# Kernel tuning notes

Measured on AMD Instinct MI355X. Metric: run time of the kernel, lower is better.

The kernel has to match this reference:

```python
import jax, jax.numpy as jnp
import numpy as np

KEEP_ID, DEL_ID, PAD_ID, STOP_ID, ANNO_ID = 1, 2, 0, 102, 103
V, E, H = 21128, 768, 768
B, T = 8, 256
S = T + 1  # org/simp length; S = T+1 guarantees counters never go out of range


def setup_inputs() -> dict:
    key = jax.random.key(0)
    ks = jax.random.split(key, 16)
    def p(i, shape, scale):
        return jax.random.normal(ks[i], shape, jnp.float32) * scale
    return {
        "input_edits": jax.random.randint(ks[0], (B, T), 0, V),
        "org_ids": jax.random.randint(ks[1], (B, S), 0, V),
        "simp_sent": jax.random.randint(ks[2], (B, S), 0, V),
        "h0": jax.random.normal(ks[3], (B, H), jnp.float32),
        "c0": jax.random.normal(ks[4], (B, H), jnp.float32),
        "encoder_outputs_org": jax.random.normal(ks[5], (B, S, E), jnp.float32),
        "emb": p(6, (V, E), 0.02),
        "Wih_e": p(7, (4 * H, E), 0.03), "Whh_e": p(8, (4 * H, H), 0.03), "b_e": jnp.zeros((4 * H,), jnp.float32),
        "Wih_w": p(9, (4 * H, E), 0.03), "Whh_w": p(10, (4 * H, H), 0.03), "b_w": jnp.zeros((4 * H,), jnp.float32),
        "W_attn": p(11, (H, H), 0.03),
        "W_align": p(12, (H, E), 0.03),
        "W_mlp": p(13, (E, 4 * H), 0.03), "b_mlp": jnp.zeros((E,), jnp.float32),
        "W_out": p(14, (V, E), 0.02), "b_out": jnp.zeros((V,), jnp.float32),
    }


def lstm(x, h0, c0, Wih, Whh, b):
    # x: [B,T,E]; single-layer batch_first LSTM, torch gate order (i,f,g,o)
    def step(carry, xt):
        h, c = carry
        g = xt @ Wih.T + h @ Whh.T + b
        i, f, gg, o = jnp.split(g, 4, axis=-1)
        c2 = jax.nn.sigmoid(f) * c + jax.nn.sigmoid(i) * jnp.tanh(gg)
        h2 = jax.nn.sigmoid(o) * jnp.tanh(c2)
        return (h2, c2), h2
    (hT, cT), hs = jax.lax.scan(step, (h0, c0), jnp.swapaxes(x, 0, 1))
    return jnp.swapaxes(hs, 0, 1), hT, cT


def reference(input_edits, org_ids, simp_sent, h0, c0, encoder_outputs_org,
              emb, Wih_e, Whh_e, b_e, Wih_w, Whh_w, b_w,
              W_attn, W_align, W_mlp, b_mlp, W_out, b_out):
    bsz, nsteps = input_edits.shape
    enc = jnp.tanh(encoder_outputs_org @ W_align.T)            # [B,S,H]
    out_edits, hT, cT = lstm(emb[input_edits], h0, c0, Wih_e, Whh_e, b_e)  # [B,T,H]
    out_words, _, _ = lstm(emb[simp_sent], h0, c0, Wih_w, Whh_w, b_w)      # [B,S,H]

    key = out_edits @ W_attn.T                                  # [B,T,H]
    attn = jax.nn.softmax(jnp.einsum('bth,bsh->bts', key, enc), axis=-1)
    ctx = jnp.einsum('bts,bsh->bth', attn, enc)                 # [B,T,H]

    # counter recurrence (pre-update counters are used for the gathers at step t)
    gold = jnp.swapaxes(input_edits[:, 1:], 0, 1)               # [T-1, B]
    bidx = jnp.arange(bsz)

    def cstep(carry, a):
        kd, ki, an = carry
        kd2 = kd + ((a == KEEP_ID) | (a == DEL_ID)).astype(kd.dtype)
        not_special = (a != DEL_ID) & (a != STOP_ID) & (a != PAD_ID)
        ki2 = ki + not_special.astype(ki.dtype)
        is_ins = not_special & (a != KEEP_ID)
        next_is_anno = org_ids[bidx, an + 1] == ANNO_ID
        an2 = jnp.where(is_ins & next_is_anno, an + 1, jnp.maximum(kd2, an))
        return (kd2, ki2, an2), (ki, an)

    z = jnp.zeros((bsz,), jnp.int32)
    _, (ki_seq, an_seq) = jax.lax.scan(cstep, (z, z, z), gold)
    ki_bt = jnp.swapaxes(ki_seq, 0, 1)                          # [B,T-1]
    an_bt = jnp.swapaxes(an_seq, 0, 1)                          # [B,T-1]

    c = jnp.take_along_axis(enc, an_bt[:, :, None], axis=1)        # [B,T-1,H]
    c_word = jnp.take_along_axis(out_words, ki_bt[:, :, None], axis=1)  # [B,T-1,H]

    Tm1 = nsteps - 1
    feat = jnp.concatenate([out_edits[:, :Tm1], ctx[:, :Tm1], c, c_word], axis=-1)  # [B,T-1,4H]
    mlp = jnp.tanh(feat @ W_mlp.T + b_mlp)                      # [B,T-1,E]
    logp = jax.nn.log_softmax(mlp @ W_out.T + b_out, axis=-1)   # [B,T-1,V]
    return logp, hT, cT
```

## Files before the change

kernel.cpp:

```cpp
#include <hip/hip_runtime.h>
#include <hip/hip_bf16.h>

typedef short s16x8 __attribute__((ext_vector_type(8)));
typedef float f32x4 __attribute__((ext_vector_type(4)));
typedef unsigned short u16;
typedef unsigned short u16x4 __attribute__((ext_vector_type(4)));
typedef unsigned long long u64;
typedef unsigned long long u64x2 __attribute__((ext_vector_type(2)));

__device__ __forceinline__ u16 f2bf(float f) {
  __hip_bfloat16 h = __float2bfloat16(f);
  u16 u;
  __builtin_memcpy(&u, &h, sizeof(u));
  return u;
}
__device__ __forceinline__ float bf2f(u16 u) {
  unsigned int x = ((unsigned int)u) << 16;
  float f;
  __builtin_memcpy(&f, &x, 4);
  return f;
}

__device__ __forceinline__ unsigned int a_ld32(const unsigned int* p) {
  return __hip_atomic_load(p, __ATOMIC_RELAXED, __HIP_MEMORY_SCOPE_AGENT);
}
__device__ __forceinline__ u64 a_ld64(const u64* p) {
  return __hip_atomic_load(p, __ATOMIC_RELAXED, __HIP_MEMORY_SCOPE_AGENT);
}
__device__ __forceinline__ void a_st32(unsigned int* p, unsigned int v) {
  __hip_atomic_store(p, v, __ATOMIC_RELAXED, __HIP_MEMORY_SCOPE_AGENT);
}

__device__ __forceinline__ void gload16(const void* g, void* l) {
  __builtin_amdgcn_global_load_lds(
      (const __attribute__((address_space(1))) unsigned int*)g,
      (__attribute__((address_space(3))) unsigned int*)l, 16, 0, 0);
}

template<int CBF16, int GATHER, int TANHA, int BIAS>
__global__ __launch_bounds__(256) void gemm_bt(
    const u16* __restrict__ A, const u16* __restrict__ B,
    const float* __restrict__ bias, void* __restrict__ Cv,
    const int* __restrict__ ids,
    int M, int N, int K, int lda, int ldb, int ldc,
    long sAz, long sBz, long sCz, int rpb, long cbs,
    const int* __restrict__ ids2, const float* __restrict__ bias2, int dM)
{
  __shared__ u16 sA[4096];
  __shared__ u16 sB[4096];
  const int tid = threadIdx.x;
  const int z = blockIdx.z;
  if (z) {
    if (dM) M += dM;
    if (ids2) ids = ids2;
    if (bias2) bias = bias2;
  }
  const int m0 = blockIdx.y * 128, n0 = blockIdx.x * 128;
  const u16* Ab = A + z * sAz;
  const u16* Bb = B + z * sBz;
  const int w = tid >> 6, lane = tid & 63;
  const int wr = w >> 1, wc = w & 1;
  const int lr = lane & 15, lk = lane >> 4;
  f32x4 acc[4][4] = {};
  const int e0 = tid * 8, e1 = e0 + 2048;
  const int r0 = e0 >> 5, c0 = e0 & 31;
  const int r1 = e1 >> 5, c1 = e1 & 31;
  long arow0, arow1;
  if (GATHER) {
    int i0 = m0 + r0; if (i0 >= M) i0 = M - 1;
    int i1 = m0 + r1; if (i1 >= M) i1 = M - 1;
    arow0 = (long)ids[i0] * lda;
    arow1 = (long)ids[i1] * lda;
  } else {
    arow0 = (long)(m0 + r0) * lda;
    arow1 = (long)(m0 + r1) * lda;
  }
  const long brow0 = (long)(n0 + r0) * ldb;
  const long brow1 = (long)(n0 + r1) * ldb;
  char* sAc = (char*)sA;
  char* sBc = (char*)sB;
  const size_t cb = (size_t)w * 1024;
  for (int kt = 0; kt < K; kt += 32) {
    __syncthreads();
    gload16(Ab + arow0 + kt + c0, sAc + cb);
    gload16(Ab + arow1 + kt + c1, sAc + 4096 + cb);
    gload16(Bb + brow0 + kt + c0, sBc + cb);
    gload16(Bb + brow1 + kt + c1, sBc + 4096 + cb);
    __syncthreads();
    s16x8 af[4], bf[4];
#pragma unroll
    for (int i = 0; i < 4; i++) {
      af[i] = *(const s16x8*)&sA[(wr*64 + i*16 + lr)*32 + lk*8];
      bf[i] = *(const s16x8*)&sB[(wc*64 + i*16 + lr)*32 + lk*8];
    }
#pragma unroll
    for (int mi = 0; mi < 4; mi++)
#pragma unroll
      for (int ni = 0; ni < 4; ni++)
        acc[mi][ni] = __builtin_amdgcn_mfma_f32_16x16x32_bf16(af[mi], bf[ni], acc[mi][ni], 0, 0, 0);
  }
#pragma unroll
  for (int mi = 0; mi < 4; mi++) {
#pragma unroll
    for (int ni = 0; ni < 4; ni++) {
#pragma unroll
      for (int r = 0; r < 4; r++) {
        int gm = m0 + wr*64 + mi*16 + lk*4 + r;
        int gn = n0 + wc*64 + ni*16 + lr;
        if (gm < M && gn < N) {
          float v = acc[mi][ni][r];
          if (BIAS) v += bias[gn];
          if (TANHA) v = tanhf(v);
          long ci = z * sCz + (long)(gm / rpb) * cbs + (long)(gm % rpb) * ldc + gn;
          if (CBF16) ((u16*)Cv)[ci] = f2bf(v);
          else       ((float*)Cv)[ci] = v;
        }
      }
    }
  }
}

__global__ __launch_bounds__(256) void cast_all(
    const float* __restrict__ emb, u16* __restrict__ emb_bf,
    const float* __restrict__ Wout, u16* __restrict__ Wout_bf,
    const float* __restrict__ Wihe, u16* __restrict__ Wihe_bf,
    const float* __restrict__ Wihw, u16* __restrict__ Wihw_bf,
    const float* __restrict__ Wmlp, u16* __restrict__ Wmlp_bf,
    const float* __restrict__ Walign, u16* __restrict__ Walign_bf,
    const float* __restrict__ Wattn, u16* __restrict__ Wattn_bf,
    const float* __restrict__ encoder, u16* __restrict__ encd_bf,
    const int* __restrict__ input_edits, const int* __restrict__ org_ids,
    int* __restrict__ ki_bt, int* __restrict__ an_bt,
    unsigned int* __restrict__ tags)
{
  int r = blockIdx.x;
  if (r == 53000) {
    int b = threadIdx.x;
    tags[b] = 0;
    if (b >= 8) return;
    int kd = 0, ki = 0, an = 0;
    for (int t = 0; t < 255; t++) {
      int a = input_edits[b * 256 + t + 1];
      ki_bt[b * 255 + t] = ki;
      an_bt[b * 255 + t] = an;
      int kd2 = kd + ((a == 1) || (a == 2) ? 1 : 0);
      int ns = (a != 2) && (a != 102) && (a != 0);
      int ki2 = ki + (ns ? 1 : 0);
      int is_ins = ns && (a != 1);
      int nia = (org_ids[b * 257 + an + 1] == 103);
      int mx = (kd2 > an) ? kd2 : an;
      int an2 = (is_ins && nia) ? (an + 1) : mx;
      kd = kd2; ki = ki2; an = an2;
    }
    return;
  }
  const float* src; u16* dst; int srows, cols;
  if (r < 21128)                    { src=emb;    dst=emb_bf;    srows=21128; cols=768; }
  else if ((r -= 21128) < 21248)    { src=Wout;   dst=Wout_bf;   srows=21128; cols=768; }
  else if ((r -= 21248) < 3072)     { src=Wihe;   dst=Wihe_bf;   srows=3072;  cols=768; }
  else if ((r -= 3072) < 3072)      { src=Wihw;   dst=Wihw_bf;   srows=3072;  cols=768; }
  else if ((r -= 3072) < 768)       { src=Wmlp;   dst=Wmlp_bf;   srows=768;   cols=3072; }
  else if ((r -= 768) < 768)        { src=Walign; dst=Walign_bf; srows=768;   cols=768; }
  else if ((r -= 768) < 768)        { src=Wattn;  dst=Wattn_bf;  srows=768;   cols=768; }
  else { r -= 768;                    src=encoder; dst=encd_bf;  srows=2056;  cols=768; }
  for (int c = threadIdx.x; c < cols; c += 256) {
    float v = (r < srows) ? src[(long)r * cols + c] : 0.f;
    dst[(long)r * cols + c] = f2bf(v);
  }
}

__global__ __launch_bounds__(256, 1) void lstm_persist(
    const float* __restrict__ Whh_e, const float* __restrict__ Whh_w,
    const float* __restrict__ xW_e, const float* __restrict__ xW_w,
    const float* __restrict__ h0, const float* __restrict__ c0,
    u16* __restrict__ hglob, unsigned int* __restrict__ tags,
    u16* __restrict__ out_e, u16* __restrict__ out_w,
    float* __restrict__ out_tail)
{
  const int wg = blockIdx.x;
  const int l = wg / 24, grp = wg % 24;
  const int u0 = grp * 32;
  const int tid = threadIdx.x;
  const int w = tid >> 6, lane = tid & 63;
  const int c16 = lane & 15, half = lane >> 4;
  const int uh = w >> 1, g0 = (w & 1) * 2;

  __shared__ u16 ldsh[12288];
  __shared__ float Gbuf[16][4][2][16];

  s16x8 wfrag[2][24];
  {
    const float* Wbase = l ? Whh_w : Whh_e;
#pragma unroll
    for (int g = 0; g < 2; g++) {
      const float* Wsrc = Wbase + (long)((g0 + g) * 768 + u0 + uh * 16 + c16) * 768 + half * 8;
#pragma unroll
      for (int s = 0; s < 24; s++) {
        float4 f0 = *(const float4*)(Wsrc + s * 32);
        float4 f1 = *(const float4*)(Wsrc + s * 32 + 4);
        s16x8 v;
        v[0]=f2bf(f0.x); v[1]=f2bf(f0.y); v[2]=f2bf(f0.z); v[3]=f2bf(f0.w);
        v[4]=f2bf(f1.x); v[5]=f2bf(f1.y); v[6]=f2bf(f1.z); v[7]=f2bf(f1.w);
        wfrag[g][s] = v;
      }
    }
  }

  const int ub = tid >> 4, j2 = (tid & 15) * 2;
  const int uA = u0 + j2;
  float creg0 = 0.f, creg1 = 0.f;
  if (tid < 128) {
    creg0 = c0[ub * 768 + uA];
    creg1 = c0[ub * 768 + uA + 1];
  }

  u16* hg = hglob + l * 24576;
  unsigned int* tg = tags + l * 64;
  const int swA = uA ^ ((ub & 7) << 3);

  if (tid < 128) {
    float v0 = h0[ub * 768 + uA], v1 = h0[ub * 768 + uA + 1];
    u16 h0a = f2bf(v0), h0b = f2bf(v1);
    u16 l0a = f2bf(v0 - bf2f(h0a)), l0b = f2bf(v1 - bf2f(h0b));
    a_st32((unsigned int*)&hg[ub * 768 + swA],
           (unsigned int)h0a | ((unsigned int)h0b << 16));
    a_st32((unsigned int*)&hg[(ub + 8) * 768 + swA],
           (unsigned int)l0a | ((unsigned int)l0b << 16));
  }
  __syncthreads();
  if (tid == 0) a_st32(&tg[grp], 1u);

  const int trow = l ? 257 : 256;
  const float* xrb = (l ? xW_w : xW_e) + ((long)ub * trow) * 3072 + uA;
  u16* outp = (l ? out_w : out_e) + (long)ub * 256 * 768 + uA;
  float2 xq0, xq1, xq2, xq3;
  if (tid < 128) {
    xq0 = *(const float2*)&xrb[0];
    xq1 = *(const float2*)&xrb[768];
    xq2 = *(const float2*)&xrb[1536];
    xq3 = *(const float2*)&xrb[2304];
  }

  for (int t = 0; t < 256; t++) {
    float2 nx0, nx1, nx2, nx3;
    if (tid < 128) {
      const float* xn = xrb + (long)(t + 1) * 3072;
      nx0 = *(const float2*)&xn[0];
      nx1 = *(const float2*)&xn[768];
      nx2 = *(const float2*)&xn[1536];
      nx3 = *(const float2*)&xn[2304];
    }

    {
      const unsigned int tgt = (unsigned int)(t + 1);
      const unsigned int* tp = tg + (t & 1) * 32;
      const bool need = (lane < 24) && (lane != grp);
      while (true) {
        unsigned int v = need ? a_ld32(&tp[lane]) : tgt;
        if (!__any(v < tgt)) break;
        __builtin_amdgcn_s_sleep(1);
      }
      asm volatile("" ::: "memory");
    }

    {
      const u64* hs8 = (const u64*)(hg + (t & 1) * 12288);
#pragma unroll
      for (int i = 0; i < 6; i++) {
        const int idx = i * 256 + tid;
        u64 a = a_ld64(&hs8[idx * 2 + 0]);
        u64 b = a_ld64(&hs8[idx * 2 + 1]);
        u64x2 vv; vv[0] = a; vv[1] = b;
        *(u64x2*)&ldsh[idx * 8] = vv;
      }
    }
    __syncthreads();

    f32x4 acc0 = {}, acc1 = {};
#pragma unroll
    for (int s = 0; s < 24; s++) {
      const int off = (c16 * 768 + s * 32 + half * 8) ^ ((c16 & 7) << 3);
      s16x8 a = *(const s16x8*)&ldsh[off];
      acc0 = __builtin_amdgcn_mfma_f32_16x16x32_bf16(a, wfrag[0][s], acc0, 0, 0, 0);
      acc1 = __builtin_amdgcn_mfma_f32_16x16x32_bf16(a, wfrag[1][s], acc1, 0, 0, 0);
    }
#pragma unroll
    for (int r = 0; r < 4; r++) {
      Gbuf[half * 4 + r][g0 + 0][uh][c16] = acc0[r];
      Gbuf[half * 4 + r][g0 + 1][uh][c16] = acc1[r];
    }
    __syncthreads();

    unsigned int hip = 0;
    float h20 = 0.f, h21 = 0.f, c20 = 0.f, c21 = 0.f;
    if (tid < 128) {
      const int uh0 = j2 >> 4, uc0 = j2 & 15;
      const int uc1 = (j2 + 1) & 15;
      float gi0 = Gbuf[ub][0][uh0][uc0] + Gbuf[ub + 8][0][uh0][uc0] + xq0.x;
      float gf0 = Gbuf[ub][1][uh0][uc0] + Gbuf[ub + 8][1][uh0][uc0] + xq1.x;
      float gg0 = Gbuf[ub][2][uh0][uc0] + Gbuf[ub + 8][2][uh0][uc0] + xq2.x;
      float go0 = Gbuf[ub][3][uh0][uc0] + Gbuf[ub + 8][3][uh0][uc0] + xq3.x;
      float gi1 = Gbuf[ub][0][uh0][uc1] + Gbuf[ub + 8][0][uh0][uc1] + xq0.y;
      float gf1 = Gbuf[ub][1][uh0][uc1] + Gbuf[ub + 8][1][uh0][uc1] + xq1.y;
      float gg1 = Gbuf[ub][2][uh0][uc1] + Gbuf[ub + 8][2][uh0][uc1] + xq2.y;
      float go1 = Gbuf[ub][3][uh0][uc1] + Gbuf[ub + 8][3][uh0][uc1] + xq3.y;
      float si0 = 1.f / (1.f + expf(-gi0)), si1 = 1.f / (1.f + expf(-gi1));
      float sf0 = 1.f / (1.f + expf(-gf0)), sf1 = 1.f / (1.f + expf(-gf1));
      float so0 = 1.f / (1.f + expf(-go0)), so1 = 1.f / (1.f + expf(-go1));
      c20 = sf0 * creg0 + si0 * tanhf(gg0);
      c21 = sf1 * creg1 + si1 * tanhf(gg1);
      h20 = so0 * tanhf(c20);
      h21 = so1 * tanhf(c21);
      creg0 = c20; creg1 = c21;
      u16 hiA = f2bf(h20), hiB = f2bf(h21);
      u16 loA = f2bf(h20 - bf2f(hiA)), loB = f2bf(h21 - bf2f(hiB));
      hip = (unsigned int)hiA | ((unsigned int)hiB << 16);
      unsigned int lop = (unsigned int)loA | ((unsigned int)loB << 16);
      u16* hb = hg + ((t + 1) & 1) * 12288;
      a_st32((unsigned int*)&hb[ub * 768 + swA], hip);
      a_st32((unsigned int*)&hb[(ub + 8) * 768 + swA], lop);
      xq0 = nx0; xq1 = nx1; xq2 = nx2; xq3 = nx3;
    }
    __syncthreads();
    if (tid == 0)
      a_st32(&tg[((t + 1) & 1) * 32 + grp], (unsigned int)(t + 2));

    if (tid < 128) {
      *(unsigned int*)&outp[(long)t * 768] = hip;
      if (l == 0 && t == 255) {
        *(float2*)&out_tail[43101120 + ub * 768 + uA] = make_float2(h20, h21);
        *(float2*)&out_tail[43107264 + ub * 768 + uA] = make_float2(c20, c21);
      }
    }
  }
}

__global__ __launch_bounds__(256) void softmax_k(
    const float* __restrict__ scores, u16* __restrict__ attn)
{
  const int row = blockIdx.x;
  const float* src = scores + (long)row * 288;
  u16* dst = attn + (long)row * 288;
  const int tid = threadIdx.x;
  float v0 = (tid < 257) ? src[tid] : -1e30f;
  float v1 = (tid + 256 < 257) ? src[tid + 256] : -1e30f;
  float mx = fmaxf(v0, v1);
  for (int o = 32; o; o >>= 1) mx = fmaxf(mx, __shfl_xor(mx, o));
  __shared__ float sm[4];
  __shared__ float ss[4];
  if ((tid & 63) == 0) sm[tid >> 6] = mx;
  __syncthreads();
  mx = fmaxf(fmaxf(sm[0], sm[1]), fmaxf(sm[2], sm[3]));
  float e0 = (tid < 257) ? expf(v0 - mx) : 0.f;
  float e1 = (tid + 256 < 257) ? expf(v1 - mx) : 0.f;
  float s = e0 + e1;
  for (int o = 32; o; o >>= 1) s += __shfl_xor(s, o);
  if ((tid & 63) == 0) ss[tid >> 6] = s;
  __syncthreads();
  s = ss[0] + ss[1] + ss[2] + ss[3];
  float inv = 1.f / s;
  dst[tid] = f2bf(e0 * inv);
  if (tid + 256 < 288) dst[tid + 256] = f2bf(e1 * inv);
}

__global__ __launch_bounds__(256) void transpose_enc(
    const u16* __restrict__ enc, u16* __restrict__ encT)
{
  __shared__ u16 tile[32][33];
  const int b = blockIdx.z, h0 = blockIdx.y * 32, s0 = blockIdx.x * 32;
  const int tx = threadIdx.x & 31, ty = threadIdx.x >> 5;
#pragma unroll
  for (int i = 0; i < 32; i += 8) {
    int s = s0 + ty + i;
    u16 v = (s < 257) ? enc[((long)b * 384 + s) * 768 + h0 + tx] : (u16)0;
    tile[ty + i][tx] = v;
  }
  __syncthreads();
#pragma unroll
  for (int i = 0; i < 32; i += 8) {
    int h = h0 + ty + i;
    encT[((long)b * 768 + h) * 288 + s0 + tx] = tile[tx][ty + i];
  }
}

__global__ __launch_bounds__(256) void feat_k(
    const u16* __restrict__ oute, const u16* __restrict__ ctx,
    const u16* __restrict__ encb, const u16* __restrict__ outw,
    const int* __restrict__ ki_bt, const int* __restrict__ an_bt,
    u16* __restrict__ feat)
{
  int q = blockIdx.x * 256 + threadIdx.x;
  int m = q / 768, qq = q - m * 768;
  int seg = qq / 192, off = (qq - seg * 192) * 4;
  u16x4 v = {0, 0, 0, 0};
  if (m < 2040) {
    int b = m / 255, t = m - b * 255;
    const u16* src;
    if (seg == 0)      src = oute + ((long)(b * 256 + t)) * 768 + off;
    else if (seg == 1) src = ctx  + ((long)(b * 256 + t)) * 768 + off;
    else if (seg == 2) src = encb + ((long)(b * 384 + an_bt[m])) * 768 + off;
    else               src = outw + ((long)(b * 256 + ki_bt[m])) * 768 + off;
    v = *(const u16x4*)src;
  }
  *(u16x4*)(feat + (long)q * 4) = v;
}

__global__ __launch_bounds__(256) void logsoftmax_k(float* __restrict__ logits)
{
  const int m = blockIdx.x;
  float* row = logits + (long)m * 21128;
  const int tid = threadIdx.x;
  float mx = -1e30f, sm = 0.f;
  for (int i = tid * 4; i < 21128; i += 1024) {
    float4 v = *(const float4*)(row + i);
    float m4 = fmaxf(fmaxf(v.x, v.y), fmaxf(v.z, v.w));
    if (m4 > mx) { sm *= expf(mx - m4); mx = m4; }
    sm += expf(v.x - mx) + expf(v.y - mx) + expf(v.z - mx) + expf(v.w - mx);
  }
  for (int o = 32; o; o >>= 1) {
    float mo = __shfl_xor(mx, o), so = __shfl_xor(sm, o);
    float nm = fmaxf(mx, mo);
    sm = sm * expf(mx - nm) + so * expf(mo - nm);
    mx = nm;
  }
  __shared__ float wm[4], wsum[4];
  __shared__ float srs;
  if ((tid & 63) == 0) { wm[tid >> 6] = mx; wsum[tid >> 6] = sm; }
  __syncthreads();
  if (tid == 0) {
    float M = wm[0], S = wsum[0];
    for (int i = 1; i < 4; i++) {
      float nm = fmaxf(M, wm[i]);
      S = S * expf(M - nm) + wsum[i] * expf(wm[i] - nm);
      M = nm;
    }
    srs = M + logf(S);
  }
  __syncthreads();
  const float rs = srs;
  for (int i = tid * 4; i < 21128; i += 1024) {
    float4 v = *(const float4*)(row + i);
    v.x -= rs; v.y -= rs; v.z -= rs; v.w -= rs;
    *(float4*)(row + i) = v;
  }
}

extern "C" void kernel_launch(void* const* d_in, const int* in_sizes, int n_in,
                              void* d_out, int out_size, void* d_ws, size_t ws_size,
                              hipStream_t stream) {
  (void)in_sizes; (void)n_in; (void)out_size; (void)ws_size;
  const int*   input_edits = (const int*)d_in[0];
  const int*   org_ids     = (const int*)d_in[1];
  const int*   simp_sent   = (const int*)d_in[2];
  const float* h0      = (const float*)d_in[3];
  const float* c0      = (const float*)d_in[4];
  const float* encoder = (const float*)d_in[5];
  const float* emb     = (const float*)d_in[6];
  const float* Wih_e   = (const float*)d_in[7];
  const float* Whh_e   = (const float*)d_in[8];
  const float* b_e     = (const float*)d_in[9];
  const float* Wih_w   = (const float*)d_in[10];
  const float* Whh_w   = (const float*)d_in[11];
  const float* b_w     = (const float*)d_in[12];
  const float* W_attn  = (const float*)d_in[13];
  const float* W_align = (const float*)d_in[14];
  const float* W_mlp   = (const float*)d_in[15];
  const float* b_mlp   = (const float*)d_in[16];
  const float* W_out   = (const float*)d_in[17];
  const float* b_out   = (const float*)d_in[18];

  float* out = (float*)d_out;
  float* xW_e = out;
  float* xW_w = out + 2048L * 3072;
  u16* emb_bf  = (u16*)(out + 2048L * 3072 + 2056L * 3072);
  u16* encd_bf = emb_bf + 21128L * 768;
  u16* feat_bf = encd_bf + 2176L * 768;

  char* p = (char*)d_ws;
  auto alloc = [&](size_t bytes) -> char* {
    char* r = p; p += (bytes + 255) & ~(size_t)255; return r;
  };
  u16* Wout_bf   = (u16*)alloc(21248L * 768 * 2);
  u16* Wihe_bf   = (u16*)alloc(3072L * 768 * 2);
  u16* Wihw_bf   = (u16*)alloc(3072L * 768 * 2);
  u16* Wmlp_bf   = (u16*)alloc(768L * 3072 * 2);
  u16* Walign_bf = (u16*)alloc(768L * 768 * 2);
  u16* Wattn_bf  = (u16*)alloc(768L * 768 * 2);
  u16* enc_bf    = (u16*)alloc(8L * 384 * 768 * 2);
  u16* encT_bf   = (u16*)alloc(8L * 768 * 288 * 2);
  u16* oute_bf   = (u16*)alloc(2048L * 768 * 2);
  u16* outw_bf   = (u16*)alloc(2048L * 768 * 2);
  u16* key_bf    = (u16*)alloc(2048L * 768 * 2);
  u16* attn_bf   = (u16*)alloc(8L * 256 * 288 * 2);
  u16* ctx_bf    = (u16*)alloc(2048L * 768 * 2);
  u16* mlp_bf    = (u16*)alloc(2048L * 768 * 2);
  float* scores  = (float*)alloc(8L * 256 * 288 * 4);
  u16* hglob     = (u16*)alloc(2L * 2 * 12288 * 2);
  unsigned int* tags = (unsigned int*)alloc(256 * 4);
  int* ki_bt     = (int*)alloc(2040 * 4);
  int* an_bt     = (int*)alloc(2040 * 4);

  dim3 blk(256);
  const int BIGR = 1 << 30;

  cast_all<<<53001, blk, 0, stream>>>(emb, emb_bf, W_out, Wout_bf,
                                      Wih_e, Wihe_bf, Wih_w, Wihw_bf,
                                      W_mlp, Wmlp_bf, W_align, Walign_bf,
                                      W_attn, Wattn_bf, encoder, encd_bf,
                                      input_edits, org_ids, ki_bt, an_bt, tags);

  gemm_bt<1, 0, 1, 0><<<dim3(6, 17, 1), blk, 0, stream>>>(
      encd_bf, Walign_bf, nullptr, enc_bf, nullptr,
      2056, 768, 768, 768, 768, 768, 0, 0, 0, 257, 294912L,
      nullptr, nullptr, 0);

  gemm_bt<0, 1, 0, 1><<<dim3(24, 17, 2), blk, 0, stream>>>(
      emb_bf, Wihe_bf, b_e, xW_e, input_edits,
      2048, 3072, 768, 768, 768, 3072, 0, 2359296L, 6291456L, BIGR, 0,
      simp_sent, b_w, 8);

  lstm_persist<<<48, blk, 0, stream>>>(
      Whh_e, Whh_w, xW_e, xW_w, h0, c0, hglob, tags,
      oute_bf, outw_bf, out);

  gemm_bt<1, 0, 0, 0><<<dim3(6, 16, 1), blk, 0, stream>>>(
      oute_bf, Wattn_bf, nullptr, key_bf, nullptr,
      2048, 768, 768, 768, 768, 768, 0, 0, 0, BIGR, 0,
      nullptr, nullptr, 0);
  gemm_bt<0, 0, 0, 0><<<dim3(3, 2, 8), blk, 0, stream>>>(
      key_bf, enc_bf, nullptr, scores, nullptr,
      256, 257, 768, 768, 768, 288, 196608L, 294912L, 73728L, BIGR, 0,
      nullptr, nullptr, 0);
  softmax_k<<<2048, blk, 0, stream>>>(scores, attn_bf);
  transpose_enc<<<dim3(9, 24, 8), blk, 0, stream>>>(enc_bf, encT_bf);
  gemm_bt<1, 0, 0, 0><<<dim3(6, 2, 8), blk, 0, stream>>>(
      attn_bf, encT_bf, nullptr, ctx_bf, nullptr,
      256, 768, 288, 288, 288, 768, 73728L, 221184L, 196608L, BIGR, 0,
      nullptr, nullptr, 0);

  feat_k<<<6144, blk, 0, stream>>>(oute_bf, ctx_bf, enc_bf, outw_bf,
                                   ki_bt, an_bt, feat_bf);
  gemm_bt<1, 0, 1, 1><<<dim3(6, 16, 1), blk, 0, stream>>>(
      feat_bf, Wmlp_bf, b_mlp, mlp_bf, nullptr,
      2040, 768, 3072, 3072, 3072, 768, 0, 0, 0, BIGR, 0,
      nullptr, nullptr, 0);
  gemm_bt<0, 0, 0, 1><<<dim3(166, 16, 1), blk, 0, stream>>>(
      mlp_bf, Wout_bf, b_out, out, nullptr,
      2040, 21128, 768, 768, 768, 21128, 0, 0, 0, BIGR, 0,
      nullptr, nullptr, 0);

  logsoftmax_k<<<2040, blk, 0, stream>>>(out);
}
```

Baseline: 1.706 ms.

## Overlap weight casts with LSTM and gather embeddings instead of casting full table

Result: faster. 1.661 ms (-2.6%).

```diff
diff --git a/kernel.cpp b/kernel.cpp
--- a/kernel.cpp
+++ b/kernel.cpp
@@ -37,7 +37,7 @@
       (__attribute__((address_space(3))) unsigned int*)l, 16, 0, 0);
 }
 
-template<int CBF16, int GATHER, int TANHA, int BIAS>
+template<int CBF16, int GATHER, int TANHA, int BIAS, int SWAPXY>
 __global__ __launch_bounds__(256) void gemm_bt(
     const u16* __restrict__ A, const u16* __restrict__ B,
     const float* __restrict__ bias, void* __restrict__ Cv,
@@ -55,7 +55,8 @@
     if (ids2) ids = ids2;
     if (bias2) bias = bias2;
   }
-  const int m0 = blockIdx.y * 128, n0 = blockIdx.x * 128;
+  const int m0 = (SWAPXY ? blockIdx.x : blockIdx.y) * 128;
+  const int n0 = (SWAPXY ? blockIdx.y : blockIdx.x) * 128;
   const u16* Ab = A + z * sAz;
   const u16* Bb = B + z * sBz;
   const int w = tid >> 6, lane = tid & 63;
@@ -120,21 +121,20 @@
   }
 }
 
-__global__ __launch_bounds__(256) void cast_all(
-    const float* __restrict__ emb, u16* __restrict__ emb_bf,
-    const float* __restrict__ Wout, u16* __restrict__ Wout_bf,
+__global__ __launch_bounds__(256) void cast_pre(
+    const float* __restrict__ emb,
     const float* __restrict__ Wihe, u16* __restrict__ Wihe_bf,
     const float* __restrict__ Wihw, u16* __restrict__ Wihw_bf,
-    const float* __restrict__ Wmlp, u16* __restrict__ Wmlp_bf,
     const float* __restrict__ Walign, u16* __restrict__ Walign_bf,
-    const float* __restrict__ Wattn, u16* __restrict__ Wattn_bf,
     const float* __restrict__ encoder, u16* __restrict__ encd_bf,
-    const int* __restrict__ input_edits, const int* __restrict__ org_ids,
+    u16* __restrict__ gath_bf,
+    const int* __restrict__ input_edits, const int* __restrict__ simp_sent,
+    const int* __restrict__ org_ids,
     int* __restrict__ ki_bt, int* __restrict__ an_bt,
     unsigned int* __restrict__ tags)
 {
   int r = blockIdx.x;
-  if (r == 53000) {
+  if (r == 13312) {
     int b = threadIdx.x;
     tags[b] = 0;
     if (b >= 8) return;
@@ -154,18 +154,18 @@
     }
     return;
   }
-  const float* src; u16* dst; int srows, cols;
-  if (r < 21128)                    { src=emb;    dst=emb_bf;    srows=21128; cols=768; }
-  else if ((r -= 21128) < 21248)    { src=Wout;   dst=Wout_bf;   srows=21128; cols=768; }
-  else if ((r -= 21248) < 3072)     { src=Wihe;   dst=Wihe_bf;   srows=3072;  cols=768; }
-  else if ((r -= 3072) < 3072)      { src=Wihw;   dst=Wihw_bf;   srows=3072;  cols=768; }
-  else if ((r -= 3072) < 768)       { src=Wmlp;   dst=Wmlp_bf;   srows=768;   cols=3072; }
-  else if ((r -= 768) < 768)        { src=Walign; dst=Walign_bf; srows=768;   cols=768; }
-  else if ((r -= 768) < 768)        { src=Wattn;  dst=Wattn_bf;  srows=768;   cols=768; }
-  else { r -= 768;                    src=encoder; dst=encd_bf;  srows=2056;  cols=768; }
+  const float* src; u16* dst; int valid, cols;
+  if (r < 3072)                   { src=Wihe + (long)r*768;   dst=Wihe_bf + (long)r*768;   valid=1; cols=768; }
+  else if ((r -= 3072) < 3072)    { src=Wihw + (long)r*768;   dst=Wihw_bf + (long)r*768;   valid=1; cols=768; }
+  else if ((r -= 3072) < 768)     { src=Walign + (long)r*768; dst=Walign_bf + (long)r*768; valid=1; cols=768; }
+  else if ((r -= 768) < 2176)     { src=encoder + (long)r*768; dst=encd_bf + (long)r*768;  valid=(r<2056); cols=768; }
+  else if ((r -= 2176) < 2048)    { src=emb + (long)input_edits[r]*768; dst=gath_bf + (long)r*768; valid=1; cols=768; }
+  else { r -= 2048;                 int ok=(r<2056);
+                                    src=emb + (ok ? (long)simp_sent[r]*768 : 0); 
+                                    dst=gath_bf + (long)(2048+r)*768; valid=ok; cols=768; }
   for (int c = threadIdx.x; c < cols; c += 256) {
-    float v = (r < srows) ? src[(long)r * cols + c] : 0.f;
-    dst[(long)r * cols + c] = f2bf(v);
+    float v = valid ? src[c] : 0.f;
+    dst[c] = f2bf(v);
   }
 }
 
@@ -175,18 +175,71 @@
     const float* __restrict__ h0, const float* __restrict__ c0,
     u16* __restrict__ hglob, unsigned int* __restrict__ tags,
     u16* __restrict__ out_e, u16* __restrict__ out_w,
-    float* __restrict__ out_tail)
+    float* __restrict__ out_tail,
+    const float* __restrict__ Wout, u16* __restrict__ Wout_bf,
+    const float* __restrict__ Wmlp, u16* __restrict__ Wmlp_bf,
+    const float* __restrict__ Wattn, u16* __restrict__ Wattn_bf,
+    const u16* __restrict__ enc_bf, u16* __restrict__ encT_bf)
 {
   const int wg = blockIdx.x;
+  const int tid = threadIdx.x;
+
+  __shared__ u16 ldsh[12288];
+  __shared__ float Gbuf[16][4][2][16];
+
+  if (wg >= 48) {
+    const int swg = wg - 48;
+    u16 (*tile)[33] = (u16(*)[33])ldsh;
+    const int TOT = 21248 + 768 + 768 + 1728;
+    for (int u = swg; u < TOT; u += 208) {
+      if (u < 21248) {
+        const float* src = Wout + (long)u * 768;
+        u16* dst = Wout_bf + (long)u * 768;
+        bool ok = (u < 21128);
+        for (int c = tid; c < 768; c += 256)
+          dst[c] = f2bf(ok ? src[c] : 0.f);
+      } else if (u < 22016) {
+        int r = u - 21248;
+        const float* src = Wmlp + (long)r * 3072;
+        u16* dst = Wmlp_bf + (long)r * 3072;
+        for (int c = tid; c < 3072; c += 256)
+          dst[c] = f2bf(src[c]);
+      } else if (u < 22784) {
+        int r = u - 22016;
+        const float* src = Wattn + (long)r * 768;
+        u16* dst = Wattn_bf + (long)r * 768;
+        for (int c = tid; c < 768; c += 256)
+          dst[c] = f2bf(src[c]);
+      } else {
+        int tau = u - 22784;
+        int s0 = (tau % 9) * 32;
+        int rem = tau / 9;
+        int hh0 = (rem % 24) * 32;
+        int b = rem / 24;
+        const int tx = tid & 31, ty = tid >> 5;
+#pragma unroll
+        for (int i = 0; i < 32; i += 8) {
+          int s = s0 + ty + i;
+          u16 v = (s < 257) ? enc_bf[((long)b * 384 + s) * 768 + hh0 + tx] : (u16)0;
+          tile[ty + i][tx] = v;
+        }
+        __syncthreads();
+#pragma unroll
+        for (int i = 0; i < 32; i += 8) {
+          int h = hh0 + ty + i;
+          encT_bf[((long)b * 768 + h) * 288 + s0 + tx] = tile[tx][ty + i];
+        }
+        __syncthreads();
+      }
+    }
+    return;
+  }
+
   const int l = wg / 24, grp = wg % 24;
   const int u0 = grp * 32;
-  const int tid = threadIdx.x;
   const int w = tid >> 6, lane = tid & 63;
   const int c16 = lane & 15, half = lane >> 4;
   const int uh = w >> 1, g0 = (w & 1) * 2;
-
-  __shared__ u16 ldsh[12288];
-  __shared__ float Gbuf[16][4][2][16];
 
   s16x8 wfrag[2][24];
   {
@@ -363,26 +416,6 @@
   if (tid + 256 < 288) dst[tid + 256] = f2bf(e1 * inv);
 }
 
-__global__ __launch_bounds__(256) void transpose_enc(
-    const u16* __restrict__ enc, u16* __restrict__ encT)
-{
-  __shared__ u16 tile[32][33];
-  const int b = blockIdx.z, h0 = blockIdx.y * 32, s0 = blockIdx.x * 32;
-  const int tx = threadIdx.x & 31, ty = threadIdx.x >> 5;
-#pragma unroll
-  for (int i = 0; i < 32; i += 8) {
-    int s = s0 + ty + i;
-    u16 v = (s < 257) ? enc[((long)b * 384 + s) * 768 + h0 + tx] : (u16)0;
-    tile[ty + i][tx] = v;
-  }
-  __syncthreads();
-#pragma unroll
-  for (int i = 0; i < 32; i += 8) {
-    int h = h0 + ty + i;
-    encT[((long)b * 768 + h) * 288 + s0 + tx] = tile[tx][ty + i];
-  }
-}
-
 __global__ __launch_bounds__(256) void feat_k(
     const u16* __restrict__ oute, const u16* __restrict__ ctx,
     const u16* __restrict__ encb, const u16* __restrict__ outw,
@@ -472,8 +505,7 @@
   float* out = (float*)d_out;
   float* xW_e = out;
   float* xW_w = out + 2048L * 3072;
-  u16* emb_bf  = (u16*)(out + 2048L * 3072 + 2056L * 3072);
-  u16* encd_bf = emb_bf + 21128L * 768;
+  u16* encd_bf = (u16*)(out + 2048L * 3072 + 2056L * 3072);
   u16* feat_bf = encd_bf + 2176L * 768;
 
   char* p = (char*)d_ws;
@@ -486,6 +518,7 @@
   u16* Wmlp_bf   = (u16*)alloc(768L * 3072 * 2);
   u16* Walign_bf = (u16*)alloc(768L * 768 * 2);
   u16* Wattn_bf  = (u16*)alloc(768L * 768 * 2);
+  u16* gath_bf   = (u16*)alloc(4224L * 768 * 2);
   u16* enc_bf    = (u16*)alloc(8L * 384 * 768 * 2);
   u16* encT_bf   = (u16*)alloc(8L * 768 * 288 * 2);
   u16* oute_bf   = (u16*)alloc(2048L * 768 * 2);
@@ -503,48 +536,47 @@
   dim3 blk(256);
   const int BIGR = 1 << 30;
 
-  cast_all<<<53001, blk, 0, stream>>>(emb, emb_bf, W_out, Wout_bf,
-                                      Wih_e, Wihe_bf, Wih_w, Wihw_bf,
-                                      W_mlp, Wmlp_bf, W_align, Walign_bf,
-                                      W_attn, Wattn_bf, encoder, encd_bf,
-                                      input_edits, org_ids, ki_bt, an_bt, tags);
-
-  gemm_bt<1, 0, 1, 0><<<dim3(6, 17, 1), blk, 0, stream>>>(
+  cast_pre<<<13313, blk, 0, stream>>>(emb, Wih_e, Wihe_bf, Wih_w, Wihw_bf,
+                                      W_align, Walign_bf, encoder, encd_bf,
+                                      gath_bf, input_edits, simp_sent,
+                                      org_ids, ki_bt, an_bt, tags);
+
+  gemm_bt<1, 0, 1, 0, 0><<<dim3(6, 17, 1), blk, 0, stream>>>(
       encd_bf, Walign_bf, nullptr, enc_bf, nullptr,
       2056, 768, 768, 768, 768, 768, 0, 0, 0, 257, 294912L,
       nullptr, nullptr, 0);
 
-  gemm_bt<0, 1, 0, 1><<<dim3(24, 17, 2), blk, 0, stream>>>(
-      emb_bf, Wihe_bf, b_e, xW_e, input_edits,
-      2048, 3072, 768, 768, 768, 3072, 0, 2359296L, 6291456L, BIGR, 0,
-      simp_sent, b_w, 8);
-
-  lstm_persist<<<48, blk, 0, stream>>>(
+  gemm_bt<0, 0, 0, 1, 0><<<dim3(24, 17, 2), blk, 0, stream>>>(
+      gath_bf, Wihe_bf, b_e, xW_e, nullptr,
+      2048, 3072, 768, 768, 768, 3072, 1572864L, 2359296L, 6291456L, BIGR, 0,
+      nullptr, b_w, 8);
+
+  lstm_persist<<<256, blk, 0, stream>>>(
       Whh_e, Whh_w, xW_e, xW_w, h0, c0, hglob, tags,
-      oute_bf, outw_bf, out);
-
-  gemm_bt<1, 0, 0, 0><<<dim3(6, 16, 1), blk, 0, stream>>>(
+      oute_bf, outw_bf, out,
+      W_out, Wout_bf, W_mlp, Wmlp_bf, W_attn, Wattn_bf, enc_bf, encT_bf);
+
+  gemm_bt<1, 0, 0, 0, 0><<<dim3(6, 16, 1), blk, 0, stream>>>(
       oute_bf, Wattn_bf, nullptr, key_bf, nullptr,
       2048, 768, 768, 768, 768, 768, 0, 0, 0, BIGR, 0,
       nullptr, nullptr, 0);
-  gemm_bt<0, 0, 0, 0><<<dim3(3, 2, 8), blk, 0, stream>>>(
+  gemm_bt<0, 0, 0, 0, 0><<<dim3(3, 2, 8), blk, 0, stream>>>(
       key_bf, enc_bf, nullptr, scores, nullptr,
       256, 257, 768, 768, 768, 288, 196608L, 294912L, 73728L, BIGR, 0,
       nullptr, nullptr, 0);
   softmax_k<<<2048, blk, 0, stream>>>(scores, attn_bf);
-  transpose_enc<<<dim3(9, 24, 8), blk, 0, stream>>>(enc_bf, encT_bf);
-  gemm_bt<1, 0, 0, 0><<<dim3(6, 2, 8), blk, 0, stream>>>(
+  gemm_bt<1, 0, 0, 0, 0><<<dim3(6, 2, 8), blk, 0, stream>>>(
       attn_bf, encT_bf, nullptr, ctx_bf, nullptr,
       256, 768, 288, 288, 288, 768, 73728L, 221184L, 196608L, BIGR, 0,
       nullptr, nullptr, 0);
 
   feat_k<<<6144, blk, 0, stream>>>(oute_bf, ctx_bf, enc_bf, outw_bf,
                                    ki_bt, an_bt, feat_bf);
-  gemm_bt<1, 0, 1, 1><<<dim3(6, 16, 1), blk, 0, stream>>>(
+  gemm_bt<1, 0, 1, 1, 0><<<dim3(6, 16, 1), blk, 0, stream>>>(
       feat_bf, Wmlp_bf, b_mlp, mlp_bf, nullptr,
       2040, 768, 3072, 3072, 3072, 768, 0, 0, 0, BIGR, 0,
       nullptr, nullptr, 0);
-  gemm_bt<0, 0, 0, 1><<<dim3(166, 16, 1), blk, 0, stream>>>(
+  gemm_bt<0, 0, 0, 1, 1><<<dim3(16, 166, 1), blk, 0, stream>>>(
       mlp_bf, Wout_bf, b_out, out, nullptr,
       2040, 21128, 768, 768, 768, 21128, 0, 0, 0, BIGR, 0,
       nullptr, nullptr, 0);
```
